# Kernel tuning notes

Measured on AMD Instinct MI355X. Metric: run time of the kernel, lower is better.

Reference implementation:

```python
import jax, jax.numpy as jnp
import numpy as np

B, T, C, H, W = 4, 8, 128, 96, 96
D = 64  # d_model

def setup_inputs() -> dict:
    key = jax.random.key(0)
    ks = jax.random.split(key, 7)
    return {
        "x": jax.random.normal(ks[0], (B, T, C, H, W), dtype=jnp.float32),
        "Wq": jax.random.normal(ks[1], (D, C), dtype=jnp.float32) * (1.0 / np.sqrt(C)),
        "bq": jax.random.normal(ks[2], (D,), dtype=jnp.float32) * 0.01,
        "Wk": jax.random.normal(ks[3], (D, C), dtype=jnp.float32) * (1.0 / np.sqrt(C)),
        "bk": jax.random.normal(ks[4], (D,), dtype=jnp.float32) * 0.01,
        "Wv": jax.random.normal(ks[5], (C, C), dtype=jnp.float32) * (1.0 / np.sqrt(C)),
        "bv": jax.random.normal(ks[6], (C,), dtype=jnp.float32) * 0.01,
    }

def reference(x, Wq, bq, Wk, bk, Wv, bv):
    # x: (B, T, C, H, W). 1x1 convs == per-pixel channel matmuls.
    d_model = Wq.shape[0]
    scale = 1.0 / jnp.sqrt(jnp.asarray(d_model, x.dtype))
    # Project and land directly in (B, H, W, T, feat) layout (fuses the permutes).
    Q = jnp.einsum('btchw,dc->bhwtd', x, Wq) + bq  # (B,H,W,T,D)
    K = jnp.einsum('btchw,dc->bhwtd', x, Wk) + bk  # (B,H,W,T,D)
    V = jnp.einsum('btchw,ec->bhwte', x, Wv) + bv  # (B,H,W,T,C)
    scores = jnp.einsum('bhwtd,bhwsd->bhwts', Q, K) * scale  # (B,H,W,T,T)
    attn = jax.nn.softmax(scores, axis=-1)
    out = jnp.einsum('bhwts,bhwse->bhwte', attn, V)  # (B,H,W,T,C)
    return jnp.transpose(out, (0, 3, 4, 1, 2))  # (B,T,C,H,W)
```

## Files before the change

### kernel.cpp

```cpp
#include <hip/hip_runtime.h>
#include <hip/hip_bf16.h>

#define TT 8
#define CC 128
#define DD 64
#define HWp 9216
#define PP 16
#define XB_STRIDE 152
#define QKV_STRIDE 264

typedef __attribute__((ext_vector_type(8))) short short8;
typedef __attribute__((ext_vector_type(4))) short short4v;
typedef __attribute__((ext_vector_type(4))) float floatx4;

__device__ __forceinline__ short f2bf(float f) {
    __hip_bfloat16 h = __float2bfloat16(f);
    return __builtin_bit_cast(short, h);
}
__device__ __forceinline__ float bf2f(short s) {
    unsigned u = ((unsigned)(unsigned short)s) << 16;
    return __builtin_bit_cast(float, u);
}

__global__ __launch_bounds__(512, 4) void ta_kernel(
    const float* __restrict__ x,
    const float* __restrict__ Wq, const float* __restrict__ bq,
    const float* __restrict__ Wk, const float* __restrict__ bk,
    const float* __restrict__ Wv, const float* __restrict__ bv,
    float* __restrict__ out)
{
    __shared__ short xb[PP * XB_STRIDE];
    __shared__ short qkv[TT * PP * QKV_STRIDE];

    const int tid  = threadIdx.x;
    const int wave = tid >> 6;
    const int lane = tid & 63;
    const int quad = lane >> 4;
    const int l16  = lane & 15;

    const int blk = blockIdx.x;
    const int b   = blk / (HWp / PP);
    const int p0  = (blk % (HWp / PP)) * PP;

    short8 wfrag[2][4];
    float  bias[2][4];
#pragma unroll
    for (int i = 0; i < 2; ++i) {
        const int f0  = (wave * 2 + i) * 16;
        const int row = f0 + l16;
        const float* wrow;
        if (row < DD)            wrow = Wq + row * CC;
        else if (row < 2 * DD)   wrow = Wk + (row - DD) * CC;
        else                     wrow = Wv + (row - 2 * DD) * CC;
#pragma unroll
        for (int kc = 0; kc < 4; ++kc) {
            const float* src = wrow + kc * 32 + quad * 8;
            short8 v;
#pragma unroll
            for (int j = 0; j < 8; ++j) v[j] = f2bf(src[j]);
            wfrag[i][kc] = v;
        }
        const int fb = f0 + quad * 4;
        const float* bsrc; int off;
        if (fb < DD)            { bsrc = bq; off = fb; }
        else if (fb < 2 * DD)   { bsrc = bk; off = fb - DD; }
        else                    { bsrc = bv; off = fb - 2 * DD; }
#pragma unroll
        for (int r = 0; r < 4; ++r) bias[i][r] = bsrc[off + r];
    }

    const int c0 = tid >> 2;
    const int p4 = (tid & 3) * 4;
    const float* xsrc0 = x + ((size_t)(b * TT) * CC + c0) * HWp + p0 + p4;

    float4 cur = *(const float4*)xsrc0;
    for (int t = 0; t < TT; ++t) {
        float4 nxt = cur;
        if (t < TT - 1)
            nxt = *(const float4*)(xsrc0 + (size_t)(t + 1) * CC * HWp);

        __syncthreads();
        xb[(p4 + 0) * XB_STRIDE + c0] = f2bf(cur.x);
        xb[(p4 + 1) * XB_STRIDE + c0] = f2bf(cur.y);
        xb[(p4 + 2) * XB_STRIDE + c0] = f2bf(cur.z);
        xb[(p4 + 3) * XB_STRIDE + c0] = f2bf(cur.w);
        __syncthreads();

        floatx4 acc[2];
#pragma unroll
        for (int i = 0; i < 2; ++i)
#pragma unroll
            for (int r = 0; r < 4; ++r) acc[i][r] = 0.f;
#pragma unroll
        for (int kc = 0; kc < 4; ++kc) {
            short8 xf = *(const short8*)&xb[l16 * XB_STRIDE + kc * 32 + quad * 8];
            acc[0] = __builtin_amdgcn_mfma_f32_16x16x32_bf16(wfrag[0][kc], xf, acc[0], 0, 0, 0);
            acc[1] = __builtin_amdgcn_mfma_f32_16x16x32_bf16(wfrag[1][kc], xf, acc[1], 0, 0, 0);
        }
#pragma unroll
        for (int i = 0; i < 2; ++i) {
            const int f0 = (wave * 2 + i) * 16 + quad * 4;
            short4v o;
#pragma unroll
            for (int r = 0; r < 4; ++r) o[r] = f2bf(acc[i][r] + bias[i][r]);
            *(short4v*)&qkv[(t * PP + l16) * QKV_STRIDE + f0] = o;
        }
        cur = nxt;
    }
    __syncthreads();

    {
        const int p  = tid & 15;
        const int g  = tid >> 4;
        const int tq = g >> 2;
        const int e0 = (g & 3) * 32;

        const short* qrow = &qkv[(tq * PP + p) * QKV_STRIDE];
        float qv[DD];
#pragma unroll
        for (int dc = 0; dc < 8; ++dc) {
            short8 v = *(const short8*)(qrow + dc * 8);
#pragma unroll
            for (int j = 0; j < 8; ++j) qv[dc * 8 + j] = bf2f(v[j]);
        }
        float sc[TT];
#pragma unroll
        for (int s = 0; s < TT; ++s) {
            const short* krow = &qkv[(s * PP + p) * QKV_STRIDE + DD];
            float a = 0.f;
#pragma unroll
            for (int dc = 0; dc < 8; ++dc) {
                short8 v = *(const short8*)(krow + dc * 8);
#pragma unroll
                for (int j = 0; j < 8; ++j) a += qv[dc * 8 + j] * bf2f(v[j]);
            }
            sc[s] = a * 0.125f;
        }
        float m = sc[0];
#pragma unroll
        for (int s = 1; s < TT; ++s) m = fmaxf(m, sc[s]);
        float sum = 0.f;
#pragma unroll
        for (int s = 0; s < TT; ++s) { sc[s] = __expf(sc[s] - m); sum += sc[s]; }
        const float inv = 1.f / sum;
#pragma unroll
        for (int s = 0; s < TT; ++s) sc[s] *= inv;

        float o[32];
#pragma unroll
        for (int j = 0; j < 32; ++j) o[j] = 0.f;
#pragma unroll
        for (int s = 0; s < TT; ++s) {
            const short* vrow = &qkv[(s * PP + p) * QKV_STRIDE + 2 * DD + e0];
            const float a = sc[s];
#pragma unroll
            for (int ec = 0; ec < 4; ++ec) {
                short8 v = *(const short8*)(vrow + ec * 8);
#pragma unroll
                for (int j = 0; j < 8; ++j) o[ec * 8 + j] += a * bf2f(v[j]);
            }
        }
        float* op = out + ((size_t)((b * TT + tq) * CC + e0)) * HWp + p0 + p;
#pragma unroll
        for (int e = 0; e < 32; ++e) op[(size_t)e * HWp] = o[e];
    }
}

extern "C" void kernel_launch(void* const* d_in, const int* in_sizes, int n_in,
                              void* d_out, int out_size, void* d_ws, size_t ws_size,
                              hipStream_t stream) {
    const float* x  = (const float*)d_in[0];
    const float* Wq = (const float*)d_in[1];
    const float* bq = (const float*)d_in[2];
    const float* Wk = (const float*)d_in[3];
    const float* bk = (const float*)d_in[4];
    const float* Wv = (const float*)d_in[5];
    const float* bv = (const float*)d_in[6];
    float* out = (float*)d_out;

    const int blocks = 4 * (HWp / PP);
    ta_kernel<<<blocks, 512, 0, stream>>>(x, Wq, bq, Wk, bk, Wv, bv, out);
}
```

Baseline: 324.7 us.

## Split QK scoring across lanes with shuffle reduction and share softmax via LDS

The attention phase is reorganized. Each wave now handles one query timestep, and each lane quad computes a 16-dim slice of the QK dot product, with the partial sums combined by cross-lane shuffles. Before, every thread recomputed all 64-dim scores redundantly. Normalized softmax weights are written once into the reused xb LDS buffer and read back by all lanes for the PV accumulation, which now uses packed float2 FMAs. The qkv buffer gets a per-timestep padded stride to change the LDS bank mapping. The cost is an extra block-wide barrier plus shuffle and LDS round-trip latency.

```diff
diff --git a/kernel.cpp b/kernel.cpp
--- a/kernel.cpp
+++ b/kernel.cpp
@@ -8,10 +8,12 @@
 #define PP 16
 #define XB_STRIDE 152
 #define QKV_STRIDE 264
+#define PS 4232
 
 typedef __attribute__((ext_vector_type(8))) short short8;
 typedef __attribute__((ext_vector_type(4))) short short4v;
 typedef __attribute__((ext_vector_type(4))) float floatx4;
+typedef __attribute__((ext_vector_type(2))) float float2v;
 
 __device__ __forceinline__ short f2bf(float f) {
     __hip_bfloat16 h = __float2bfloat16(f);
@@ -30,7 +32,7 @@
     float* __restrict__ out)
 {
     __shared__ short xb[PP * XB_STRIDE];
-    __shared__ short qkv[TT * PP * QKV_STRIDE];
+    __shared__ short qkv[TT * PS];
 
     const int tid  = threadIdx.x;
     const int wave = tid >> 6;
@@ -103,38 +105,45 @@
             short4v o;
 #pragma unroll
             for (int r = 0; r < 4; ++r) o[r] = f2bf(acc[i][r] + bias[i][r]);
-            *(short4v*)&qkv[(t * PP + l16) * QKV_STRIDE + f0] = o;
+            *(short4v*)&qkv[t * PS + l16 * QKV_STRIDE + f0] = o;
         }
         cur = nxt;
     }
     __syncthreads();
 
+    float* attn = (float*)xb;
+
     {
-        const int p  = tid & 15;
-        const int g  = tid >> 4;
-        const int tq = g >> 2;
-        const int e0 = (g & 3) * 32;
-
-        const short* qrow = &qkv[(tq * PP + p) * QKV_STRIDE];
-        float qv[DD];
-#pragma unroll
-        for (int dc = 0; dc < 8; ++dc) {
-            short8 v = *(const short8*)(qrow + dc * 8);
-#pragma unroll
-            for (int j = 0; j < 8; ++j) qv[dc * 8 + j] = bf2f(v[j]);
+        const int p  = l16;
+        const int dq = quad;
+        const int tq = wave;
+
+        const short* qp = &qkv[tq * PS + p * QKV_STRIDE + dq * 16];
+        float qv[16];
+        {
+            short8 q0 = *(const short8*)qp;
+            short8 q1 = *(const short8*)(qp + 8);
+#pragma unroll
+            for (int j = 0; j < 8; ++j) { qv[j] = bf2f(q0[j]); qv[8 + j] = bf2f(q1[j]); }
         }
         float sc[TT];
 #pragma unroll
         for (int s = 0; s < TT; ++s) {
-            const short* krow = &qkv[(s * PP + p) * QKV_STRIDE + DD];
+            const short* kp = &qkv[s * PS + p * QKV_STRIDE + DD + dq * 16];
+            short8 k0 = *(const short8*)kp;
+            short8 k1 = *(const short8*)(kp + 8);
             float a = 0.f;
 #pragma unroll
-            for (int dc = 0; dc < 8; ++dc) {
-                short8 v = *(const short8*)(krow + dc * 8);
-#pragma unroll
-                for (int j = 0; j < 8; ++j) a += qv[dc * 8 + j] * bf2f(v[j]);
-            }
-            sc[s] = a * 0.125f;
+            for (int j = 0; j < 8; ++j) a += qv[j] * bf2f(k0[j]);
+#pragma unroll
+            for (int j = 0; j < 8; ++j) a += qv[8 + j] * bf2f(k1[j]);
+            sc[s] = a;
+        }
+#pragma unroll
+        for (int s = 0; s < TT; ++s) {
+            sc[s] += __shfl_xor(sc[s], 16);
+            sc[s] += __shfl_xor(sc[s], 32);
+            sc[s] *= 0.125f;
         }
         float m = sc[0];
 #pragma unroll
@@ -143,26 +152,50 @@
 #pragma unroll
         for (int s = 0; s < TT; ++s) { sc[s] = __expf(sc[s] - m); sum += sc[s]; }
         const float inv = 1.f / sum;
-#pragma unroll
-        for (int s = 0; s < TT; ++s) sc[s] *= inv;
-
-        float o[32];
-#pragma unroll
-        for (int j = 0; j < 32; ++j) o[j] = 0.f;
+        if (dq == 0) {
+            float* ap = &attn[(tq * PP + p) * 8];
+#pragma unroll
+            for (int s = 0; s < TT; ++s) ap[s] = sc[s] * inv;
+        }
+    }
+    __syncthreads();
+
+    {
+        const int p  = l16;
+        const int eq = quad;
+        const int tq = wave;
+
+        float w[TT];
+        {
+            const float4 wa = *(const float4*)&attn[(tq * PP + p) * 8];
+            const float4 wb = *(const float4*)&attn[(tq * PP + p) * 8 + 4];
+            w[0]=wa.x; w[1]=wa.y; w[2]=wa.z; w[3]=wa.w;
+            w[4]=wb.x; w[5]=wb.y; w[6]=wb.z; w[7]=wb.w;
+        }
+        float2v o2[16];
+#pragma unroll
+        for (int k = 0; k < 16; ++k) { o2[k][0] = 0.f; o2[k][1] = 0.f; }
 #pragma unroll
         for (int s = 0; s < TT; ++s) {
-            const short* vrow = &qkv[(s * PP + p) * QKV_STRIDE + 2 * DD + e0];
-            const float a = sc[s];
-#pragma unroll
-            for (int ec = 0; ec < 4; ++ec) {
-                short8 v = *(const short8*)(vrow + ec * 8);
-#pragma unroll
-                for (int j = 0; j < 8; ++j) o[ec * 8 + j] += a * bf2f(v[j]);
+            const short* vp = &qkv[s * PS + p * QKV_STRIDE + 2 * DD + eq * 32];
+            const float a = w[s];
+            const float2v a2 = { a, a };
+#pragma unroll
+            for (int c = 0; c < 4; ++c) {
+                short8 v = *(const short8*)(vp + c * 8);
+#pragma unroll
+                for (int j = 0; j < 4; ++j) {
+                    float2v f = { bf2f(v[2 * j]), bf2f(v[2 * j + 1]) };
+                    o2[c * 4 + j] += a2 * f;
+                }
             }
         }
-        float* op = out + ((size_t)((b * TT + tq) * CC + e0)) * HWp + p0 + p;
-#pragma unroll
-        for (int e = 0; e < 32; ++e) op[(size_t)e * HWp] = o[e];
+        float* op = out + ((size_t)((b * TT + tq) * CC + eq * 32)) * HWp + p0 + p;
+#pragma unroll
+        for (int k = 0; k < 16; ++k) {
+            op[(size_t)(2 * k) * HWp]     = o2[k][0];
+            op[(size_t)(2 * k + 1) * HWp] = o2[k][1];
+        }
     }
 }
 
```

After: 339.3 us. 1.04x slower.
